# Performance work log

Measured on AMD Instinct MI355X. Metric: run time of the kernel, lower is better.

Reference implementation:

```python
import jax, jax.numpy as jnp
import numpy as np

NCLS = 21
HW = 41  # featUpsample target size


def setup_inputs() -> dict:
    key = jax.random.key(0)
    ks = jax.random.split(key, 8)
    x = jax.random.normal(ks[0], (4, 2048, 33, 33), dtype=jnp.float32)
    diffW = jax.random.uniform(ks[1], (4, HW * HW, HW * HW), dtype=jnp.float32)
    # conv weights init normal(0, 0.01) as in the torch module
    conv_w = jax.random.normal(ks[2], (1024, 2048, 3, 3), dtype=jnp.float32) * 0.01
    conv_b = jnp.zeros((1024,), jnp.float32)
    cls_w = jax.random.normal(ks[3], (NCLS, 1024, 1, 1), dtype=jnp.float32) * 0.01
    cls_b = jnp.zeros((NCLS,), jnp.float32)
    sm_scale_w = jnp.ones((1, NCLS), jnp.float32) * 1.5   # softMax_scale.weights
    pool_w = jnp.ones((1, NCLS), jnp.float32) * 5.0       # weiPooling.weights
    ms_scales = jnp.array([0.95, 0.75, 0.6, 0.4], jnp.float32)
    return {"x": x, "diffW": diffW, "conv_w": conv_w, "conv_b": conv_b,
            "cls_w": cls_w, "cls_b": cls_b, "sm_scale_w": sm_scale_w,
            "pool_w": pool_w, "ms_scales": ms_scales}


def reference(x, diffW, conv_w, conv_b, cls_w, cls_b, sm_scale_w, pool_w, ms_scales):
    bs = x.shape[0]
    # bilinear upsample to 41x41 (align_corners=False semantics, same as jax.image.resize)
    x = jax.image.resize(x, (bs, x.shape[1], HW, HW), method="bilinear")
    # ASPP branch 0: dilated 3x3 conv, dilation=padding=6 keeps 41x41
    feat = jax.lax.conv_general_dilated(
        x, conv_w, window_strides=(1, 1), padding=((6, 6), (6, 6)),
        rhs_dilation=(6, 6), dimension_numbers=("NCHW", "OIHW", "NCHW"))
    feat = feat + conv_b[None, :, None, None]          # [bs,1024,41,41]
    d = feat.shape[1]
    wh = HW * HW
    f2 = feat.reshape(bs, d, wh)                        # [bs,1024,wh]
    cw = cls_w.reshape(NCLS, d)                         # 1x1 conv weight

    logits = []
    for it in range(4):
        cs = (diffW > ms_scales[it]).astype(f2.dtype)   # [bs,wh,wh]
        # diag(1/rowsum) @ cs, then transpose -> column-normalized-after-transpose
        norm = (cs / cs.sum(axis=2, keepdims=True)).transpose(0, 2, 1)
        od = jnp.einsum("bdn,bnm->bdm", f2, norm)       # diffusion-smoothed features
        logits.append(jnp.einsum("bdm,cd->bcm", od, cw) + cls_b[None, :, None])
    wei_cum = jnp.stack(logits, axis=1)                 # [bs,4,ncls,wh]

    # softMax_scale: softmax over the scale (ns) axis of scaled logits
    wei_mask = jax.nn.softmax(sm_scale_w.reshape(1, 1, NCLS, 1) * wei_cum, axis=1)
    wei_cum2 = jax.nn.softmax((wei_cum * wei_mask).sum(axis=1), axis=1)  # [bs,ncls,wh]

    # weiPooling
    wei = jax.nn.softmax(wei_cum2, axis=1)
    w2 = jax.nn.softmax(wei * jnp.exp(pool_w[0]).reshape(1, NCLS, 1), axis=2)
    pooled = jnp.einsum("bcm,bdm->bcd", w2, f2)         # [bs,ncls,1024]

    # pred_sw with the 1x1 classifier weights
    out = (pooled * cw[None]).sum(axis=2) + cls_b[None]  # [bs,ncls]
    prob = jax.nn.sigmoid(out).reshape(bs, 1, NCLS)
    return (prob, wei_cum2, wei, wei_mask)
```

## Files before the change

kernel.cpp:

```cpp
#include <hip/hip_runtime.h>
#include <hip/hip_bf16.h>
#include <math.h>

#define NCLS 21
#define WH 1681
#define WHP 1684
#define BS 4
#define CIN 2048
#define NSRC 1089
#define KPOS 18432
#define MR 192
#define HS 836352
#define NT 53
#define NZ 8
#define PSLAB (16L * 22L * WHP)
#define MKZ 4
#define MSLAB (32L * KPOS)

typedef __attribute__((ext_vector_type(8))) __bf16 bf16x8;
typedef __attribute__((ext_vector_type(4))) float f32x4;

#define WS_KC    393216L
#define WS_H2    393248L
#define WS_WCUM  (WS_H2 + 4L * HS)
#define WS_G     (WS_WCUM + 564816L)
#define WS_GSW   (WS_G + 141204L)
#define WS_CF    (WS_GSW + 108544L)
#define WS_W2P   (WS_CF + 591712L)
#define WS_W2MB  (WS_W2P + 6193152L)

static __device__ __forceinline__ unsigned short f2bf(float v) {
    unsigned int b = __float_as_uint(v);
    b += 0x7FFFu + ((b >> 16) & 1u);
    return (unsigned short)(b >> 16);
}


__global__ void k_cpack(const float* __restrict__ clsw, unsigned short* __restrict__ cf) {
    int gid = blockIdx.x * blockDim.x + threadIdx.x;
    if (gid >= 32 * 2 * 64) return;
    int lane = gid & 63;
    int rt = (gid >> 6) & 1;
    int kc = gid >> 7;
    int cl = lane & 15, kg = lane >> 4;
    int c = rt * 16 + cl;
    unsigned short o[8];
#pragma unroll
    for (int j = 0; j < 8; ++j) {
        int d = kc * 32 + kg * 8 + j;
        o[j] = (c < NCLS) ? f2bf(clsw[c * 1024 + d]) : (unsigned short)0;
    }
    unsigned short* p = cf + (long)gid * 8;
#pragma unroll
    for (int j = 0; j < 8; ++j) p[j] = o[j];
}

__global__ __launch_bounds__(256) void k_mergemm(const unsigned short* __restrict__ cf,
                                                 const float* __restrict__ convw,
                                                 float* __restrict__ pmrg) {
    __shared__ unsigned short Bs[2][64][40];
    int tid = threadIdx.x;
    int lane = tid & 63, wv = tid >> 6;
    int kg = lane >> 4, cl = lane & 15;
    int pos0 = blockIdx.x * 64;
    int kz = blockIdx.y;

    const float* cb = convw + (long)(kz * 256) * KPOS + pos0 + lane;

    f32x4 acc[2];
#pragma unroll
    for (int i = 0; i < 2; ++i) acc[i] = (f32x4){0.f, 0.f, 0.f, 0.f};

    for (int ch = 0; ch < 8; ++ch) {
        const float* cc = cb + (long)(ch * 32 + wv * 8) * KPOS;
        float xr[8];
#pragma unroll
        for (int jj = 0; jj < 8; ++jj) xr[jj] = cc[(long)jj * KPOS];
        bf16x8 afr[2];
        const unsigned short* ab = cf + (((long)(kz * 8 + ch) * 2) * 64 + lane) * 8;
#pragma unroll
        for (int i = 0; i < 2; ++i) afr[i] = *(const bf16x8*)(ab + (long)i * 64 * 8);
        union { unsigned short u[8]; bf16x8 v; } bw;
#pragma unroll
        for (int jj = 0; jj < 8; ++jj) bw.u[jj] = f2bf(xr[jj]);
        int buf = ch & 1;
        *(bf16x8*)&Bs[buf][lane][wv * 8] = bw.v;
        __syncthreads();
        bf16x8 bf = *(const bf16x8*)&Bs[buf][wv * 16 + cl][kg * 8];
#pragma unroll
        for (int i = 0; i < 2; ++i)
            acc[i] = __builtin_amdgcn_mfma_f32_16x16x32_bf16(afr[i], bf, acc[i], 0, 0, 0);
        __syncthreads();
    }
    float* pz = pmrg + (long)kz * MSLAB;
    int pos = pos0 + wv * 16 + cl;
#pragma unroll
    for (int i = 0; i < 2; ++i) {
#pragma unroll
        for (int rr = 0; rr < 4; ++rr) {
            int c = i * 16 + 4 * kg + rr;
            pz[(long)c * KPOS + pos] = acc[i][rr];
        }
    }
}

__global__ void k_mfinpack(const float* __restrict__ pmrg, unsigned short* __restrict__ w2mb) {
    int gid = blockIdx.x * blockDim.x + threadIdx.x;
    if (gid >= 64 * 12 * 64) return;
    int lane = gid & 63;
    int rt = (gid >> 6) % 12;
    int kc = gid / (64 * 12);
    int cl = lane & 15, kg = lane >> 4;
    int r = rt * 16 + cl;
    unsigned short o[8];
    if (r < 189) {
        int c = r / 9, t = r - c * 9;
        const float* base = pmrg + (long)c * KPOS + t;
#pragma unroll
        for (int j = 0; j < 8; ++j) {
            int i = kc * 32 + kg * 8 + j;
            long pos = (long)i * 9;
            float s = 0.f;
#pragma unroll
            for (int kz = 0; kz < MKZ; ++kz) s += base[(long)kz * MSLAB + pos];
            o[j] = f2bf(s);
        }
    } else {
#pragma unroll
        for (int j = 0; j < 8; ++j) o[j] = 0;
    }
    unsigned short* p = w2mb + (long)gid * 8;
#pragma unroll
    for (int j = 0; j < 8; ++j) p[j] = o[j];
}

__global__ void k_const(const float* __restrict__ clsw, const float* __restrict__ convb,
                        const float* __restrict__ clsb, float* __restrict__ Kc) {
    __shared__ float red[256];
    int c = blockIdx.x;
    float s = 0.f;
    for (int d = threadIdx.x; d < 1024; d += 256) s += clsw[c * 1024 + d] * convb[d];
    red[threadIdx.x] = s; __syncthreads();
    for (int o = 128; o > 0; o >>= 1) {
        if (threadIdx.x < o) red[threadIdx.x] += red[threadIdx.x + o];
        __syncthreads();
    }
    if (threadIdx.x == 0) Kc[c] = red[0] + clsb[c];
}

__global__ __launch_bounds__(256) void k_gemmm(const unsigned short* __restrict__ w2mb,
                                               const float* __restrict__ x,
                                               float* __restrict__ Hp) {
    __shared__ unsigned short Bs[2][64][40];
    int tid = threadIdx.x;
    int lane = tid & 63, wv = tid >> 6;
    int kg = lane >> 4, cl = lane & 15;
    int n0 = blockIdx.x * 64;
    int b  = blockIdx.y;
    int ks = blockIdx.z;

    const float* xb = x + ((long)b * CIN + ks * 512) * NSRC + n0 + lane;
    bool nok = (n0 + lane) < NSRC;

    f32x4 acc[3][4];
#pragma unroll
    for (int i = 0; i < 3; ++i)
#pragma unroll
        for (int ct = 0; ct < 4; ++ct) acc[i][ct] = (f32x4){0.f, 0.f, 0.f, 0.f};

    for (int ch = 0; ch < 16; ++ch) {
        const float* xc = xb + (long)(ch * 32 + wv * 8) * NSRC;
        float xr[8];
#pragma unroll
        for (int jj = 0; jj < 8; ++jj) xr[jj] = nok ? xc[(long)jj * NSRC] : 0.f;
        bf16x8 afr[3];
        const unsigned short* wb = w2mb + (((long)(ks * 16 + ch) * 12 + wv * 3) * 64 + lane) * 8;
#pragma unroll
        for (int i = 0; i < 3; ++i) afr[i] = *(const bf16x8*)(wb + (long)i * 64 * 8);
        union { unsigned short u[8]; bf16x8 v; } bw;
#pragma unroll
        for (int jj = 0; jj < 8; ++jj) bw.u[jj] = f2bf(xr[jj]);
        int buf = ch & 1;
        *(bf16x8*)&Bs[buf][lane][wv * 8] = bw.v;
        __syncthreads();
#pragma unroll
        for (int ct = 0; ct < 4; ++ct) {
            bf16x8 bf = *(const bf16x8*)&Bs[buf][ct * 16 + cl][kg * 8];
#pragma unroll
            for (int i = 0; i < 3; ++i)
                acc[i][ct] = __builtin_amdgcn_mfma_f32_16x16x32_bf16(afr[i], bf, acc[i][ct], 0, 0, 0);
        }
        __syncthreads();
    }
    float* Hb = Hp + (long)ks * HS + (long)b * MR * NSRC;
#pragma unroll
    for (int i = 0; i < 3; ++i) {
        int r0 = (wv * 3 + i) * 16 + 4 * kg;
#pragma unroll
        for (int ct = 0; ct < 4; ++ct) {
            int n = n0 + ct * 16 + cl;
            if (n < NSRC) {
#pragma unroll
                for (int rr = 0; rr < 4; ++rr)
                    Hb[(long)(r0 + rr) * NSRC + n] = acc[i][ct][rr];
            }
        }
    }
}

__global__ void k_combine(const float* __restrict__ Hp, float* __restrict__ g) {
    int gid = blockIdx.x * blockDim.x + threadIdx.x;
    if (gid >= BS * NCLS * WH) return;
    int m = gid % WH;
    int t_ = gid / WH;
    int c = t_ % NCLS;
    int b = t_ / NCLS;
    int yy = m / 41, xx = m - yy * 41;
    const float S = 33.0f / 41.0f;
    int y0a[3], y1a[3], x0a[3], x1a[3];
    float wya[3], wxa[3];
    bool oky[3], okx[3];
#pragma unroll
    for (int o = 0; o < 3; ++o) {
        int yp = yy + 6 * o - 6;
        oky[o] = (yp >= 0 && yp < 41);
        float sy = (yp + 0.5f) * S - 0.5f;
        float fy = floorf(sy);
        wya[o] = sy - fy;
        int y0 = (int)fy;
        y0a[o] = min(max(y0, 0), 32);
        y1a[o] = min(max(y0 + 1, 0), 32);
        int xp = xx + 6 * o - 6;
        okx[o] = (xp >= 0 && xp < 41);
        float sx = (xp + 0.5f) * S - 0.5f;
        float fx = floorf(sx);
        wxa[o] = sx - fx;
        int x0 = (int)fx;
        x0a[o] = min(max(x0, 0), 32);
        x1a[o] = min(max(x0 + 1, 0), 32);
    }
    float acc = 0.f;
    const float* Hb = Hp + ((long)b * MR + c * 9) * NSRC;
#pragma unroll
    for (int ty = 0; ty < 3; ++ty) {
#pragma unroll
        for (int tx = 0; tx < 3; ++tx) {
            if (oky[ty] && okx[tx]) {
                const float* hr = Hb + (ty * 3 + tx) * NSRC;
                int i00 = y0a[ty] * 33 + x0a[tx], i01 = y0a[ty] * 33 + x1a[tx];
                int i10 = y1a[ty] * 33 + x0a[tx], i11 = y1a[ty] * 33 + x1a[tx];
                float v00 = 0.f, v01 = 0.f, v10 = 0.f, v11 = 0.f;
#pragma unroll
                for (int s = 0; s < 4; ++s) {
                    const float* h2 = hr + (long)s * HS;
                    v00 += h2[i00]; v01 += h2[i01]; v10 += h2[i10]; v11 += h2[i11];
                }
                float wy = wya[ty], wx = wxa[tx];
                float v0 = v00 + wx * (v01 - v00);
                float v1 = v10 + wx * (v11 - v10);
                acc += v0 + wy * (v1 - v0);
            }
        }
    }
    g[gid] = acc;
}

__global__ void k_gpack(const float* __restrict__ g, unsigned short* __restrict__ Gsw) {
    int gid = blockIdx.x * blockDim.x + threadIdx.x;
    if (gid >= BS * NT * 2 * 64) return;
    int lane = gid & 63;
    int t = gid >> 6;
    int ct = t & 1; t >>= 1;
    int nt = t % NT;
    int b  = t / NT;
    int col = ct * 16 + (lane & 15);
    int nb = nt * 32 + (lane >> 4) * 8;
    unsigned short out[8];
#pragma unroll
    for (int j = 0; j < 8; ++j) {
        int n = nb + j;
        unsigned short v = 0;
        if (n < WH) {
            if (col < NCLS) v = f2bf(g[((long)b * NCLS + col) * WH + n]);
            else if (col == NCLS) v = 0x3F80;
        }
        out[j] = v;
    }
    unsigned short* p = Gsw + (long)gid * 8;
#pragma unroll
    for (int j = 0; j < 8; ++j) p[j] = out[j];
}

__global__ __launch_bounds__(256) void k_dgemm(const float* __restrict__ diffW,
                                               const unsigned short* __restrict__ Gsw,
                                               const float* __restrict__ msc,
                                               float* __restrict__ pacc) {
    int tid  = threadIdx.x;
    int lane = tid & 63, wv = tid >> 6;
    int b = blockIdx.y, z = blockIdx.z;
    int m0w = blockIdx.x * 64 + wv * 16;
    int kg = lane >> 4;
    int cl = lane & 15;
    int mA = m0w + cl; if (mA > WH - 1) mA = WH - 1;
    float thr[4];
#pragma unroll
    for (int it = 0; it < 4; ++it) thr[it] = msc[it];
    int nt0 = (z * NT) / NZ;
    int nt1 = ((z + 1) * NT) / NZ;
    const float* drow = diffW + ((long)b * WH + mA) * WH;
    const unsigned short* gb = Gsw + (long)b * NT * 2 * 64 * 8;

    f32x4 accv[4][2];
#pragma unroll
    for (int it = 0; it < 4; ++it)
#pragma unroll
        for (int ct = 0; ct < 2; ++ct) accv[it][ct] = (f32x4){0.f, 0.f, 0.f, 0.f};

    for (int nt = nt0; nt < nt1; ++nt) {
        int nb = nt * 32 + kg * 8;
        float dw[8];
        if (nb + 7 <= WH - 1) {
#pragma unroll
            for (int j = 0; j < 8; ++j) dw[j] = drow[nb + j];
        } else {
#pragma unroll
            for (int j = 0; j < 8; ++j) dw[j] = (nb + j < WH) ? drow[nb + j] : -1e30f;
        }
        union { unsigned short u[8]; bf16x8 v; } af[4];
#pragma unroll
        for (int it = 0; it < 4; ++it)
#pragma unroll
            for (int j = 0; j < 8; ++j)
                af[it].u[j] = (dw[j] > thr[it]) ? (unsigned short)0x3F80 : (unsigned short)0;

        const unsigned short* gp = gb + ((long)nt * 2 * 64 + lane) * 8;
        bf16x8 b0 = *(const bf16x8*)gp;
        bf16x8 b1 = *(const bf16x8*)(gp + 64 * 8);
#pragma unroll
        for (int it = 0; it < 4; ++it) {
            accv[it][0] = __builtin_amdgcn_mfma_f32_16x16x32_bf16(af[it].v, b0, accv[it][0], 0, 0, 0);
            accv[it][1] = __builtin_amdgcn_mfma_f32_16x16x32_bf16(af[it].v, b1, accv[it][1], 0, 0, 0);
        }
    }
    float* pz = pacc + (long)z * PSLAB;
    int mbase = m0w + 4 * kg;
#pragma unroll
    for (int it = 0; it < 4; ++it) {
#pragma unroll
        for (int ct = 0; ct < 2; ++ct) {
            int c = ct * 16 + cl;
            if (c < 22) {
                float* dst = pz + ((long)(b * 4 + it) * 22 + c) * WHP + mbase;
                if (mbase + 3 < WH) {
                    *(f32x4*)dst = accv[it][ct];
                } else {
#pragma unroll
                    for (int r = 0; r < 4; ++r)
                        if (mbase + r < WH) dst[r] = accv[it][ct][r];
                }
            }
        }
    }
}

__global__ void k_dfin(const float* __restrict__ pacc, const float* __restrict__ Kc,
                       float* __restrict__ wcum) {
    int gid = blockIdx.x * blockDim.x + threadIdx.x;
    if (gid >= BS * 4 * NCLS * WH) return;
    int m = gid % WH;
    int t = gid / WH;
    int c = t % NCLS; t /= NCLS;
    int it = t & 3;
    int b = t >> 2;
    long rowc = ((long)(b * 4 + it) * 22 + c) * WHP + m;
    long rown = ((long)(b * 4 + it) * 22 + NCLS) * WHP + m;
    float num = 0.f, cnt = 0.f;
#pragma unroll
    for (int z = 0; z < NZ; ++z) {
        num += pacc[(long)z * PSLAB + rowc];
        cnt += pacc[(long)z * PSLAB + rown];
    }
    wcum[(((long)b * 4 + it) * NCLS + c) * WH + m] = num / cnt + Kc[c];
}

__global__ void k_mask(const float* __restrict__ wcum, const float* __restrict__ smw,
                       float* __restrict__ out_wc2, float* __restrict__ out_wei,
                       float* __restrict__ out_mask) {
    int gid = blockIdx.x * blockDim.x + threadIdx.x;
    if (gid >= BS * WH) return;
    int b = gid / WH, m = gid - b * WH;
    const float* base = wcum + (long)b * 4 * NCLS * WH + m;

    float fused[21];
#pragma unroll
    for (int c = 0; c < NCLS; ++c) {
        float sc = smw[c];
        float L0 = base[(0 * NCLS + c) * WH];
        float L1 = base[(1 * NCLS + c) * WH];
        float L2 = base[(2 * NCLS + c) * WH];
        float L3 = base[(3 * NCLS + c) * WH];
        float a0 = sc * L0, a1 = sc * L1, a2 = sc * L2, a3 = sc * L3;
        float mx = fmaxf(fmaxf(a0, a1), fmaxf(a2, a3));
        float e0 = __expf(a0 - mx), e1 = __expf(a1 - mx), e2 = __expf(a2 - mx), e3 = __expf(a3 - mx);
        float inv = 1.0f / (e0 + e1 + e2 + e3);
        e0 *= inv; e1 *= inv; e2 *= inv; e3 *= inv;
        out_mask[((long)(b * 4 + 0) * NCLS + c) * WH + m] = e0;
        out_mask[((long)(b * 4 + 1) * NCLS + c) * WH + m] = e1;
        out_mask[((long)(b * 4 + 2) * NCLS + c) * WH + m] = e2;
        out_mask[((long)(b * 4 + 3) * NCLS + c) * WH + m] = e3;
        fused[c] = L0 * e0 + L1 * e1 + L2 * e2 + L3 * e3;
    }
    float mx = -1e30f;
#pragma unroll
    for (int c = 0; c < NCLS; ++c) mx = fmaxf(mx, fused[c]);
    float s = 0.f;
    float e[21];
#pragma unroll
    for (int c = 0; c < NCLS; ++c) { e[c] = __expf(fused[c] - mx); s += e[c]; }
    float inv = 1.0f / s;
#pragma unroll
    for (int c = 0; c < NCLS; ++c) {
        e[c] *= inv;
        out_wc2[((long)b * NCLS + c) * WH + m] = e[c];
    }
    mx = -1e30f;
#pragma unroll
    for (int c = 0; c < NCLS; ++c) mx = fmaxf(mx, e[c]);
    s = 0.f;
    float e2a[21];
#pragma unroll
    for (int c = 0; c < NCLS; ++c) { e2a[c] = __expf(e[c] - mx); s += e2a[c]; }
    inv = 1.0f / s;
#pragma unroll
    for (int c = 0; c < NCLS; ++c) out_wei[((long)b * NCLS + c) * WH + m] = e2a[c] * inv;
}

__global__ void k_pool(const float* __restrict__ wei, const float* __restrict__ g,
                       const float* __restrict__ poolw, const float* __restrict__ Kc,
                       float* __restrict__ prob) {
    int c = blockIdx.x, b = blockIdx.y;
    const float* wr = wei + ((long)b * NCLS + c) * WH;
    const float* gr = g + ((long)b * NCLS + c) * WH;
    float E = __expf(poolw[c]);
    __shared__ float red[256];
    float mx = -1e30f;
    for (int m = threadIdx.x; m < WH; m += 256) mx = fmaxf(mx, wr[m] * E);
    red[threadIdx.x] = mx; __syncthreads();
    for (int o = 128; o > 0; o >>= 1) {
        if (threadIdx.x < o) red[threadIdx.x] = fmaxf(red[threadIdx.x], red[threadIdx.x + o]);
        __syncthreads();
    }
    mx = red[0]; __syncthreads();
    float se = 0.f, sg = 0.f;
    for (int m = threadIdx.x; m < WH; m += 256) {
        float ev = __expf(wr[m] * E - mx);
        se += ev; sg += ev * gr[m];
    }
    red[threadIdx.x] = se; __syncthreads();
    for (int o = 128; o > 0; o >>= 1) {
        if (threadIdx.x < o) red[threadIdx.x] += red[threadIdx.x + o];
        __syncthreads();
    }
    se = red[0]; __syncthreads();
    red[threadIdx.x] = sg; __syncthreads();
    for (int o = 128; o > 0; o >>= 1) {
        if (threadIdx.x < o) red[threadIdx.x] += red[threadIdx.x + o];
        __syncthreads();
    }
    sg = red[0];
    if (threadIdx.x == 0) {
        float out = sg / se + Kc[c];
        prob[b * NCLS + c] = 1.0f / (1.0f + __expf(-out));
    }
}

extern "C" void kernel_launch(void* const* d_in, const int* in_sizes, int n_in,
                              void* d_out, int out_size, void* d_ws, size_t ws_size,
                              hipStream_t stream) {
    const float* x      = (const float*)d_in[0];
    const float* diffW  = (const float*)d_in[1];
    const float* conv_w = (const float*)d_in[2];
    const float* conv_b = (const float*)d_in[3];
    const float* cls_w  = (const float*)d_in[4];
    const float* cls_b  = (const float*)d_in[5];
    const float* smw    = (const float*)d_in[6];
    const float* poolw  = (const float*)d_in[7];
    const float* msc    = (const float*)d_in[8];

    float* ws   = (float*)d_ws;
    float* Kc   = ws + WS_KC;
    float* Hp   = ws + WS_H2;
    float* wcum = ws + WS_WCUM;
    float* g    = ws + WS_G;
    unsigned short* Gsw  = (unsigned short*)(ws + WS_GSW);
    unsigned short* cf   = (unsigned short*)(ws + WS_CF);
    float* pmrg = ws + WS_W2P;
    float* pacc = ws + WS_W2P;
    unsigned short* w2mb = (unsigned short*)(ws + WS_W2MB);

    float* out  = (float*)d_out;
    float* o_prob = out;
    float* o_wc2  = out + 84;
    float* o_wei  = out + 84 + 141204;
    float* o_mask = out + 84 + 141204 + 141204;

    k_cpack<<<(32 * 2 * 64 + 255) / 256, 256, 0, stream>>>(cls_w, cf);
    k_mergemm<<<dim3(KPOS / 64, MKZ), 256, 0, stream>>>(cf, conv_w, pmrg);
    k_mfinpack<<<(64 * 12 * 64 + 255) / 256, 256, 0, stream>>>(pmrg, w2mb);
    k_const<<<NCLS, 256, 0, stream>>>(cls_w, conv_b, cls_b, Kc);
    k_gemmm<<<dim3(18, BS, 4), 256, 0, stream>>>(w2mb, x, Hp);
    k_combine<<<(BS * NCLS * WH + 255) / 256, 256, 0, stream>>>(Hp, g);
    k_gpack<<<(BS * NT * 2 * 64 + 255) / 256, 256, 0, stream>>>(g, Gsw);
    k_dgemm<<<dim3(27, BS, NZ), 256, 0, stream>>>(diffW, Gsw, msc, pacc);
    k_dfin<<<(BS * 4 * NCLS * WH + 255) / 256, 256, 0, stream>>>(pacc, Kc, wcum);
    k_mask<<<(BS * WH + 255) / 256, 256, 0, stream>>>(wcum, smw, o_wc2, o_wei, o_mask);
    k_pool<<<dim3(NCLS, BS), 256, 0, stream>>>(o_wei, g, poolw, Kc, o_prob);
}
```

Measured before the change: 98.90 us.

## Merge prep kernels, drop trailing barriers, stage diffW tile through LDS

Merges the classifier-weight pack and bias-constant kernels into one launch to save a kernel launch. Removes the second __syncthreads in the two double-buffered GEMM loops, relying on the alternating LDS buffers to avoid write-after-read hazards. Changes the diffusion GEMM to load diffW rows with coalesced 32-wide column reads into a double-buffered LDS tile, instead of strided per-lane row reads. This adds LDS traffic and a barrier per iteration, and the single-barrier double buffering could race if warps drift two iterations apart.

```diff
diff --git a/kernel.cpp b/kernel.cpp
--- a/kernel.cpp
+++ b/kernel.cpp
@@ -36,23 +36,37 @@
 }
 
 
-__global__ void k_cpack(const float* __restrict__ clsw, unsigned short* __restrict__ cf) {
-    int gid = blockIdx.x * blockDim.x + threadIdx.x;
-    if (gid >= 32 * 2 * 64) return;
-    int lane = gid & 63;
-    int rt = (gid >> 6) & 1;
-    int kc = gid >> 7;
-    int cl = lane & 15, kg = lane >> 4;
-    int c = rt * 16 + cl;
-    unsigned short o[8];
-#pragma unroll
-    for (int j = 0; j < 8; ++j) {
-        int d = kc * 32 + kg * 8 + j;
-        o[j] = (c < NCLS) ? f2bf(clsw[c * 1024 + d]) : (unsigned short)0;
-    }
-    unsigned short* p = cf + (long)gid * 8;
-#pragma unroll
-    for (int j = 0; j < 8; ++j) p[j] = o[j];
+__global__ void k_prep(const float* __restrict__ clsw, const float* __restrict__ convb,
+                       const float* __restrict__ clsb, unsigned short* __restrict__ cf,
+                       float* __restrict__ Kc) {
+    if (blockIdx.x < 16) {
+        int gid = blockIdx.x * 256 + threadIdx.x;
+        int lane = gid & 63;
+        int rt = (gid >> 6) & 1;
+        int kc = gid >> 7;
+        int cl = lane & 15, kg = lane >> 4;
+        int c = rt * 16 + cl;
+        unsigned short o[8];
+#pragma unroll
+        for (int j = 0; j < 8; ++j) {
+            int d = kc * 32 + kg * 8 + j;
+            o[j] = (c < NCLS) ? f2bf(clsw[c * 1024 + d]) : (unsigned short)0;
+        }
+        unsigned short* p = cf + (long)gid * 8;
+#pragma unroll
+        for (int j = 0; j < 8; ++j) p[j] = o[j];
+    } else {
+        __shared__ float red[256];
+        int c = blockIdx.x - 16;
+        float s = 0.f;
+        for (int d = threadIdx.x; d < 1024; d += 256) s += clsw[c * 1024 + d] * convb[d];
+        red[threadIdx.x] = s; __syncthreads();
+        for (int o = 128; o > 0; o >>= 1) {
+            if (threadIdx.x < o) red[threadIdx.x] += red[threadIdx.x + o];
+            __syncthreads();
+        }
+        if (threadIdx.x == 0) Kc[c] = red[0] + clsb[c];
+    }
 }
 
 __global__ __launch_bounds__(256) void k_mergemm(const unsigned short* __restrict__ cf,
@@ -90,7 +104,6 @@
 #pragma unroll
         for (int i = 0; i < 2; ++i)
             acc[i] = __builtin_amdgcn_mfma_f32_16x16x32_bf16(afr[i], bf, acc[i], 0, 0, 0);
-        __syncthreads();
     }
     float* pz = pmrg + (long)kz * MSLAB;
     int pos = pos0 + wv * 16 + cl;
@@ -134,20 +147,6 @@
     for (int j = 0; j < 8; ++j) p[j] = o[j];
 }
 
-__global__ void k_const(const float* __restrict__ clsw, const float* __restrict__ convb,
-                        const float* __restrict__ clsb, float* __restrict__ Kc) {
-    __shared__ float red[256];
-    int c = blockIdx.x;
-    float s = 0.f;
-    for (int d = threadIdx.x; d < 1024; d += 256) s += clsw[c * 1024 + d] * convb[d];
-    red[threadIdx.x] = s; __syncthreads();
-    for (int o = 128; o > 0; o >>= 1) {
-        if (threadIdx.x < o) red[threadIdx.x] += red[threadIdx.x + o];
-        __syncthreads();
-    }
-    if (threadIdx.x == 0) Kc[c] = red[0] + clsb[c];
-}
-
 __global__ __launch_bounds__(256) void k_gemmm(const unsigned short* __restrict__ w2mb,
                                                const float* __restrict__ x,
                                                float* __restrict__ Hp) {
@@ -190,7 +189,6 @@
             for (int i = 0; i < 3; ++i)
                 acc[i][ct] = __builtin_amdgcn_mfma_f32_16x16x32_bf16(afr[i], bf, acc[i][ct], 0, 0, 0);
         }
-        __syncthreads();
     }
     float* Hb = Hp + (long)ks * HS + (long)b * MR * NSRC;
 #pragma unroll
@@ -295,19 +293,28 @@
                                                const unsigned short* __restrict__ Gsw,
                                                const float* __restrict__ msc,
                                                float* __restrict__ pacc) {
+    __shared__ float Ds[2][64][36];
     int tid  = threadIdx.x;
     int lane = tid & 63, wv = tid >> 6;
     int b = blockIdx.y, z = blockIdx.z;
-    int m0w = blockIdx.x * 64 + wv * 16;
+    int m0 = blockIdx.x * 64;
+    int m0w = m0 + wv * 16;
     int kg = lane >> 4;
     int cl = lane & 15;
-    int mA = m0w + cl; if (mA > WH - 1) mA = WH - 1;
     float thr[4];
 #pragma unroll
     for (int it = 0; it < 4; ++it) thr[it] = msc[it];
     int nt0 = (z * NT) / NZ;
     int nt1 = ((z + 1) * NT) / NZ;
-    const float* drow = diffW + ((long)b * WH + mA) * WH;
+
+    int scol = tid & 31;
+    int srow = tid >> 5;
+    long rb[8];
+#pragma unroll
+    for (int p = 0; p < 8; ++p) {
+        int mr = m0 + srow + 8 * p; if (mr > WH - 1) mr = WH - 1;
+        rb[p] = ((long)b * WH + mr) * WH;
+    }
     const unsigned short* gb = Gsw + (long)b * NT * 2 * 64 * 8;
 
     f32x4 accv[4][2];
@@ -317,15 +324,23 @@
         for (int ct = 0; ct < 2; ++ct) accv[it][ct] = (f32x4){0.f, 0.f, 0.f, 0.f};
 
     for (int nt = nt0; nt < nt1; ++nt) {
-        int nb = nt * 32 + kg * 8;
+        int nb = nt * 32;
+        int buf = nt & 1;
+        int ncol = nb + scol;
+        if (ncol <= WH - 1) {
+#pragma unroll
+            for (int p = 0; p < 8; ++p) Ds[buf][srow + 8 * p][scol] = diffW[rb[p] + ncol];
+        } else {
+#pragma unroll
+            for (int p = 0; p < 8; ++p) Ds[buf][srow + 8 * p][scol] = -1e30f;
+        }
+        __syncthreads();
+
         float dw[8];
-        if (nb + 7 <= WH - 1) {
-#pragma unroll
-            for (int j = 0; j < 8; ++j) dw[j] = drow[nb + j];
-        } else {
-#pragma unroll
-            for (int j = 0; j < 8; ++j) dw[j] = (nb + j < WH) ? drow[nb + j] : -1e30f;
-        }
+        const float* dsr = &Ds[buf][wv * 16 + cl][kg * 8];
+#pragma unroll
+        for (int j = 0; j < 8; ++j) dw[j] = dsr[j];
+
         union { unsigned short u[8]; bf16x8 v; } af[4];
 #pragma unroll
         for (int it = 0; it < 4; ++it)
@@ -504,10 +519,9 @@
     float* o_wei  = out + 84 + 141204;
     float* o_mask = out + 84 + 141204 + 141204;
 
-    k_cpack<<<(32 * 2 * 64 + 255) / 256, 256, 0, stream>>>(cls_w, cf);
+    k_prep<<<37, 256, 0, stream>>>(cls_w, conv_b, cls_b, cf, Kc);
     k_mergemm<<<dim3(KPOS / 64, MKZ), 256, 0, stream>>>(cf, conv_w, pmrg);
     k_mfinpack<<<(64 * 12 * 64 + 255) / 256, 256, 0, stream>>>(pmrg, w2mb);
-    k_const<<<NCLS, 256, 0, stream>>>(cls_w, conv_b, cls_b, Kc);
     k_gemmm<<<dim3(18, BS, 4), 256, 0, stream>>>(w2mb, x, Hp);
     k_combine<<<(BS * NCLS * WH + 255) / 256, 256, 0, stream>>>(Hp, g);
     k_gpack<<<(BS * NT * 2 * 64 + 255) / 256, 256, 0, stream>>>(g, Gsw);
```

Measured after the change: 95.76 us. -3.2%, faster.
